# Kernel optimization log

Hardware: AMD Instinct MI355X
Metric: run time of the kernel (lower is better)

The kernel has to match this reference:

```python
import jax, jax.numpy as jnp
import numpy as np

VOCAB = 100000; E = 256; H = 256; Hh = 128; K = 12
START = 9; STOP = 10; PAD = 11; NEG = -10000.0
B = 32; T = 512


def setup_inputs() -> dict:
    key = jax.random.key(0)
    ks = jax.random.split(key, 16)
    u = 1.0 / np.sqrt(Hh)  # pytorch LSTM init scale
    xav = lambda k, shape: jax.random.normal(k, shape, jnp.float32) * np.sqrt(2.0 / (shape[0] + shape[1]))
    trans = jax.random.normal(ks[10], (K, K), jnp.float32)
    trans = trans.at[START, :].set(NEG).at[:, STOP].set(NEG)
    trans = trans.at[PAD, :].set(NEG).at[:, PAD].set(NEG)
    return {
        "sentence": jax.random.randint(ks[0], (B, T), 0, VOCAB),
        "h0": jax.random.normal(ks[1], (2, B, Hh), jnp.float32),
        "c0": jax.random.normal(ks[2], (2, B, Hh), jnp.float32),
        "embed": xav(ks[3], (VOCAB, E)),
        "W_ih_f": jax.random.uniform(ks[4], (4 * Hh, E), jnp.float32, -u, u),
        "W_hh_f": jax.random.uniform(ks[5], (4 * Hh, Hh), jnp.float32, -u, u),
        "b_f": jax.random.uniform(ks[6], (4 * Hh,), jnp.float32, -u, u),
        "W_ih_r": jax.random.uniform(ks[7], (4 * Hh, E), jnp.float32, -u, u),
        "W_hh_r": jax.random.uniform(ks[8], (4 * Hh, Hh), jnp.float32, -u, u),
        "b_r": jax.random.uniform(ks[9], (4 * Hh,), jnp.float32, -u, u),
        "W_out": xav(ks[11], (K, H)),
        "b_out": jnp.zeros((K,), jnp.float32),
        "transitions": trans,
    }


def _lstm_dir(xe, W_ih, W_hh, b, h0, c0):
    # xe: [T,B,E]; precompute input contribution once (big GEMM outside scan)
    xg = jnp.einsum('tbe,ge->tbg', xe, W_ih) + b  # [T,B,4*Hh]
    def step(carry, xt):
        h, c = carry
        g = xt + h @ W_hh.T
        i, f, gg, o = jnp.split(g, 4, axis=-1)  # pytorch gate order i,f,g,o
        c = jax.nn.sigmoid(f) * c + jax.nn.sigmoid(i) * jnp.tanh(gg)
        h = jax.nn.sigmoid(o) * jnp.tanh(c)
        return (h, c), h
    _, hs = jax.lax.scan(step, (h0, c0), xg)
    return hs  # [T,B,Hh]


def reference(sentence, h0, c0, embed, W_ih_f, W_hh_f, b_f, W_ih_r, W_hh_r, b_r,
              W_out, b_out, transitions):
    xe = embed[sentence].transpose(1, 0, 2)  # [T,B,E]
    hs_f = _lstm_dir(xe, W_ih_f, W_hh_f, b_f, h0[0], c0[0])
    hs_r = _lstm_dir(xe[::-1], W_ih_r, W_hh_r, b_r, h0[1], c0[1])[::-1]
    hs = jnp.concatenate([hs_f, hs_r], axis=-1)           # [T,B,H]
    feats = hs @ W_out.T + b_out                          # [T,B,K]

    # Viterbi max-plus recurrence
    scores0 = jnp.full((B, K), NEG, jnp.float32).at[:, START].set(0.0)
    def vstep(scores, feat):
        m = scores[:, None, :] + transitions[None, :, :]  # [B,K_next,K_prev]
        ptr = jnp.argmax(m, axis=-1).astype(jnp.int32)
        return jnp.max(m, axis=-1) + feat, ptr
    scores, pointers = jax.lax.scan(vstep, scores0, feats)  # pointers [T,B,K]
    scores = scores + transitions[STOP]
    best_tag = jnp.argmax(scores, axis=-1).astype(jnp.int32)  # [B]

    # parallel backtrace (reverse scan, outputs in original time order)
    def back(tag, ptr):
        prev = jnp.take_along_axis(ptr, tag[:, None], axis=1)[:, 0]
        return prev, tag
    _, path = jax.lax.scan(back, best_tag, pointers, reverse=True)  # [T,B]
    return path.T  # [B,T] int32 best tag sequence
```

## Files before the change

### kernel.cpp

```cpp
#include <hip/hip_runtime.h>
#include <hip/hip_bf16.h>
#include <cmath>

#define TT 512
#define BB 32
#define EE 256
#define HH 128
#define KCRF 12
#define NEGF (-10000.0f)

__global__ __launch_bounds__(256) void k1_xg(const int* __restrict__ sent,
    const float* __restrict__ embed,
    const float* __restrict__ Wf, const float* __restrict__ bf,
    const float* __restrict__ Wr, const float* __restrict__ br,
    float* __restrict__ XG)
{
  __shared__ __align__(16) float As[64][36];
  __shared__ __align__(16) float Bs[128][36];
  const int tid = threadIdx.x;
  const int m0 = (blockIdx.x >> 3) * 64;
  const int n0 = (blockIdx.x & 7) * 128;
  const int ty = tid >> 4, tx = tid & 15;
  float acc[4][8];
#pragma unroll
  for (int i = 0; i < 4; ++i)
#pragma unroll
    for (int j = 0; j < 8; ++j) acc[i][j] = 0.f;

  for (int k0 = 0; k0 < 256; k0 += 32) {
#pragma unroll
    for (int r = 0; r < 2; ++r) {
      int idx = tid + r * 256;
      int row = idx >> 3;
      int c4 = (idx & 7) << 2;
      int R = m0 + row;
      int t = R >> 5, b = R & 31;
      const float4 v = *(const float4*)(embed + (long)sent[b * TT + t] * 256 + k0 + c4);
      *(float4*)&As[row][c4] = v;
    }
#pragma unroll
    for (int r = 0; r < 4; ++r) {
      int idx = tid + r * 256;
      int row = idx >> 3;
      int c4 = (idx & 7) << 2;
      int col = n0 + row;
      const float* src = (col < 512) ? (Wf + (long)col * 256) : (Wr + (long)(col - 512) * 256);
      const float4 v = *(const float4*)(src + k0 + c4);
      *(float4*)&Bs[row][c4] = v;
    }
    __syncthreads();
#pragma unroll
    for (int kk = 0; kk < 32; ++kk) {
      float a[4], bv[8];
#pragma unroll
      for (int i = 0; i < 4; ++i) a[i] = As[ty * 4 + i][kk];
#pragma unroll
      for (int j = 0; j < 8; ++j) bv[j] = Bs[tx + 16 * j][kk];
#pragma unroll
      for (int i = 0; i < 4; ++i)
#pragma unroll
        for (int j = 0; j < 8; ++j) acc[i][j] = fmaf(a[i], bv[j], acc[i][j]);
    }
    __syncthreads();
  }
#pragma unroll
  for (int i = 0; i < 4; ++i) {
    int R = m0 + ty * 4 + i;
#pragma unroll
    for (int j = 0; j < 8; ++j) {
      int col = n0 + tx + 16 * j;
      float bias = (col < 512) ? bf[col] : br[col - 512];
      XG[(long)R * 1024 + col] = acc[i][j] + bias;
    }
  }
}

__global__ __launch_bounds__(512) __attribute__((amdgpu_waves_per_eu(1)))
void k2_scan(const float* __restrict__ XG,
    const float* __restrict__ Whf, const float* __restrict__ Whr,
    const float* __restrict__ h0, const float* __restrict__ c0,
    float* __restrict__ HS)
{
  const int wg = blockIdx.x;
  const int dir = wg >> 5;
  const int b = wg & 31;
  const int j = threadIdx.x;
  const float* Wh = dir ? Whr : Whf;

  float4 w[32];
#pragma unroll
  for (int i = 0; i < 32; ++i)
    w[i] = *(const float4*)(Wh + (long)j * 128 + i * 4);

  __shared__ __align__(16) float hs[128];
  __shared__ float gs[512];
  float c = 0.f;
  if (j < 128) {
    hs[j] = h0[(dir * 32 + b) * 128 + j];
    c = c0[(dir * 32 + b) * 128 + j];
  }
  __syncthreads();

  const int t0 = dir ? (TT - 1) : 0;
  const long stepoff = dir ? -32768 : 32768;
  const float* xp = XG + ((long)t0 * 32 + b) * 1024 + dir * 512 + j;
  float xg_cur = *xp;
  const int gate = j >> 7;

  for (int s = 0; s < TT; ++s) {
    const int t = dir ? (TT - 1 - s) : s;
    float xg_nxt = 0.f;
    if (s + 1 < TT) { xp += stepoff; xg_nxt = *xp; }

    float a0 = xg_cur, a1 = 0.f, a2 = 0.f, a3 = 0.f;
#pragma unroll
    for (int i = 0; i < 32; ++i) {
      const float4 hv = *(const float4*)(hs + 4 * i);
      a0 = fmaf(w[i].x, hv.x, a0);
      a1 = fmaf(w[i].y, hv.y, a1);
      a2 = fmaf(w[i].z, hv.z, a2);
      a3 = fmaf(w[i].w, hv.w, a3);
    }
    const float acc = (a0 + a1) + (a2 + a3);
    const float act = (gate == 2) ? tanhf(acc) : (1.f / (1.f + expf(-acc)));
    gs[j] = act;
    __syncthreads();
    if (j < 128) {
      float ig = gs[j], fg = gs[128 + j], gg = gs[256 + j], og = gs[384 + j];
      c = fmaf(fg, c, ig * gg);
      float h = og * tanhf(c);
      hs[j] = h;
      HS[((long)t * 32 + b) * 256 + dir * 128 + j] = h;
    }
    __syncthreads();
    xg_cur = xg_nxt;
  }
}

__global__ __launch_bounds__(64) void k3_feats(const float* __restrict__ HS,
    const float* __restrict__ Wout, const float* __restrict__ bout,
    float* __restrict__ FE)
{
  __shared__ __align__(16) float ws[12 * 256];
  __shared__ float bs[12];
  const int tid = threadIdx.x;
  for (int i = tid; i < 768; i += 64)
    ((float4*)ws)[i] = ((const float4*)Wout)[i];
  if (tid < 12) bs[tid] = bout[tid];
  __syncthreads();
  const long row = (long)blockIdx.x * 64 + tid;
  const float4* hp = (const float4*)(HS + row * 256);
  float acc[12];
#pragma unroll
  for (int k = 0; k < 12; ++k) acc[k] = bs[k];
  for (int e4 = 0; e4 < 64; ++e4) {
    float4 hv = hp[e4];
#pragma unroll
    for (int k = 0; k < 12; ++k) {
      const float4 wv = *(const float4*)&ws[k * 256 + e4 * 4];
      acc[k] = fmaf(hv.x, wv.x, acc[k]);
      acc[k] = fmaf(hv.y, wv.y, acc[k]);
      acc[k] = fmaf(hv.z, wv.z, acc[k]);
      acc[k] = fmaf(hv.w, wv.w, acc[k]);
    }
  }
  const int t = (int)(row >> 5), b = (int)(row & 31);
#pragma unroll
  for (int k = 0; k < 12; ++k) FE[((long)t * 12 + k) * 32 + b] = acc[k];
}

__global__ __launch_bounds__(384) void k4_viterbi(const float* __restrict__ FE,
    const float* __restrict__ trans, int* __restrict__ out)
{
  __shared__ unsigned char nib[TT * 192];
  __shared__ float sc[2][32][12];
  __shared__ float tr[144];
  __shared__ unsigned char stag[2][384];
  __shared__ int btag[32];
  const int tid = threadIdx.x;
  const int b = tid & 31, nxt = tid >> 5;
  if (tid < 144) tr[tid] = trans[tid];
  if (nxt == 0) {
#pragma unroll
    for (int p = 0; p < 12; ++p) sc[0][b][p] = (p == 9) ? 0.f : NEGF;
  }
  __syncthreads();
  float fnext = FE[nxt * 32 + b];
  for (int t = 0; t < TT; ++t) {
    const int cur = t & 1;
    const float feat = fnext;
    if (t + 1 < TT) fnext = FE[(t + 1) * 384 + nxt * 32 + b];
    float best = -1e30f; int arg = 0;
#pragma unroll
    for (int p = 0; p < 12; ++p) {
      float v = sc[cur][b][p] + tr[nxt * 12 + p];
      if (v > best) { best = v; arg = p; }
    }
    sc[cur ^ 1][b][nxt] = best + feat;
    stag[cur][b * 12 + nxt] = (unsigned char)arg;
    if (t > 0 && tid < 192) {
      const int bb = tid / 6, p = tid % 6;
      nib[(t - 1) * 192 + tid] =
          (unsigned char)(stag[cur ^ 1][bb * 12 + 2 * p] |
                          (stag[cur ^ 1][bb * 12 + 2 * p + 1] << 4));
    }
    __syncthreads();
  }
  if (tid < 192) {
    const int bb = tid / 6, p = tid % 6;
    nib[511 * 192 + tid] =
        (unsigned char)(stag[1][bb * 12 + 2 * p] | (stag[1][bb * 12 + 2 * p + 1] << 4));
  }
  if (nxt == 0) {
    float best = -1e30f; int arg = 0;
#pragma unroll
    for (int p = 0; p < 12; ++p) {
      float v = sc[0][b][p] + tr[10 * 12 + p];
      if (v > best) { best = v; arg = p; }
    }
    btag[b] = arg;
  }
  __syncthreads();
  if (tid < 32) {
    int tag = btag[b];
    for (int t = TT - 1; t >= 0; --t) {
      out[b * TT + t] = tag;
      if (t) {
        unsigned char v = nib[t * 192 + b * 6 + (tag >> 1)];
        tag = (tag & 1) ? (v >> 4) : (v & 15);
      }
    }
  }
}

extern "C" void kernel_launch(void* const* d_in, const int* in_sizes, int n_in,
                              void* d_out, int out_size, void* d_ws, size_t ws_size,
                              hipStream_t stream)
{
  const int* sent = (const int*)d_in[0];
  const float* h0 = (const float*)d_in[1];
  const float* c0 = (const float*)d_in[2];
  const float* embed = (const float*)d_in[3];
  const float* Wif = (const float*)d_in[4];
  const float* Whf = (const float*)d_in[5];
  const float* bf = (const float*)d_in[6];
  const float* Wir = (const float*)d_in[7];
  const float* Whr = (const float*)d_in[8];
  const float* br = (const float*)d_in[9];
  const float* Wout = (const float*)d_in[10];
  const float* bout = (const float*)d_in[11];
  const float* trans = (const float*)d_in[12];

  char* ws = (char*)d_ws;
  float* XG = (float*)ws;
  float* HS = (float*)(ws + 67108864);
  float* FE = (float*)(ws + 67108864 + 16777216);
  int* out = (int*)d_out;

  hipLaunchKernelGGL(k1_xg, dim3(2048), dim3(256), 0, stream,
                     sent, embed, Wif, bf, Wir, br, XG);
  hipLaunchKernelGGL(k2_scan, dim3(64), dim3(512), 0, stream,
                     XG, Whf, Whr, h0, c0, HS);
  hipLaunchKernelGGL(k3_feats, dim3(256), dim3(64), 0, stream,
                     HS, Wout, bout, FE);
  hipLaunchKernelGGL(k4_viterbi, dim3(1), dim3(384), 0, stream,
                     FE, trans, out);
}
```

Before: 809.5 us.

## Process two batch rows per LSTM scan workgroup to reuse register weights

The recurrent LSTM kernel now handles two batch elements per workgroup, so each thread's register-resident W_hh row is applied to two hidden vectors per step. This halves the grid from 64 to 32 workgroups and doubles the FMA work per thread per step. The barrier count per step stays the same but is shared across two sequences. The gain depends on whether per-step latency is set by barriers and the activation and LDS path rather than by FMA throughput, and the smaller grid leaves more CUs idle.

Result: slower. 1.880 ms (+132.3%).

```diff
diff --git a/kernel.cpp b/kernel.cpp
--- a/kernel.cpp
+++ b/kernel.cpp
@@ -75,65 +75,85 @@
   }
 }
 
-__global__ __launch_bounds__(512) __attribute__((amdgpu_waves_per_eu(1)))
+__global__ __launch_bounds__(512, 2)
 void k2_scan(const float* __restrict__ XG,
     const float* __restrict__ Whf, const float* __restrict__ Whr,
     const float* __restrict__ h0, const float* __restrict__ c0,
     float* __restrict__ HS)
 {
   const int wg = blockIdx.x;
-  const int dir = wg >> 5;
-  const int b = wg & 31;
+  const int dir = wg >> 4;
+  const int b1 = wg & 15;
+  const int b2 = b1 + 16;
   const int j = threadIdx.x;
   const float* Wh = dir ? Whr : Whf;
 
   float4 w[32];
 #pragma unroll
   for (int i = 0; i < 32; ++i)
-    w[i] = *(const float4*)(Wh + (long)j * 128 + i * 4);
-
-  __shared__ __align__(16) float hs[128];
-  __shared__ float gs[512];
+    w[i] = *(const float4*)(Wh + (long)j * 128 + 4 * i);
+
+  __shared__ __align__(16) float hs[2][128];
+  __shared__ float gs[2][512];
   float c = 0.f;
   if (j < 128) {
-    hs[j] = h0[(dir * 32 + b) * 128 + j];
-    c = c0[(dir * 32 + b) * 128 + j];
+    hs[0][j] = h0[(dir * 32 + b1) * 128 + j];
+    c = c0[(dir * 32 + b1) * 128 + j];
+  } else if (j < 256) {
+    hs[1][j - 128] = h0[(dir * 32 + b2) * 128 + (j - 128)];
+    c = c0[(dir * 32 + b2) * 128 + (j - 128)];
   }
   __syncthreads();
 
   const int t0 = dir ? (TT - 1) : 0;
   const long stepoff = dir ? -32768 : 32768;
-  const float* xp = XG + ((long)t0 * 32 + b) * 1024 + dir * 512 + j;
-  float xg_cur = *xp;
+  const float* xp1 = XG + ((long)t0 * 32 + b1) * 1024 + dir * 512 + j;
+  const float* xp2 = XG + ((long)t0 * 32 + b2) * 1024 + dir * 512 + j;
+  float xg1 = *xp1, xg2 = *xp2;
   const int gate = j >> 7;
 
   for (int s = 0; s < TT; ++s) {
     const int t = dir ? (TT - 1 - s) : s;
-    float xg_nxt = 0.f;
-    if (s + 1 < TT) { xp += stepoff; xg_nxt = *xp; }
-
-    float a0 = xg_cur, a1 = 0.f, a2 = 0.f, a3 = 0.f;
+    float nx1 = 0.f, nx2 = 0.f;
+    if (s + 1 < TT) {
+      xp1 += stepoff; nx1 = *xp1;
+      xp2 += stepoff; nx2 = *xp2;
+    }
+
+    float a0 = xg1, a1 = 0.f, a2 = 0.f, a3 = 0.f;
+    float d0 = xg2, d1 = 0.f, d2 = 0.f, d3 = 0.f;
 #pragma unroll
     for (int i = 0; i < 32; ++i) {
-      const float4 hv = *(const float4*)(hs + 4 * i);
-      a0 = fmaf(w[i].x, hv.x, a0);
-      a1 = fmaf(w[i].y, hv.y, a1);
-      a2 = fmaf(w[i].z, hv.z, a2);
-      a3 = fmaf(w[i].w, hv.w, a3);
-    }
-    const float acc = (a0 + a1) + (a2 + a3);
-    const float act = (gate == 2) ? tanhf(acc) : (1.f / (1.f + expf(-acc)));
-    gs[j] = act;
-    __syncthreads();
-    if (j < 128) {
-      float ig = gs[j], fg = gs[128 + j], gg = gs[256 + j], og = gs[384 + j];
+      const float4 h1 = *(const float4*)(hs[0] + 4 * i);
+      const float4 h2 = *(const float4*)(hs[1] + 4 * i);
+      a0 = fmaf(w[i].x, h1.x, a0);
+      a1 = fmaf(w[i].y, h1.y, a1);
+      a2 = fmaf(w[i].z, h1.z, a2);
+      a3 = fmaf(w[i].w, h1.w, a3);
+      d0 = fmaf(w[i].x, h2.x, d0);
+      d1 = fmaf(w[i].y, h2.y, d1);
+      d2 = fmaf(w[i].z, h2.z, d2);
+      d3 = fmaf(w[i].w, h2.w, d3);
+    }
+    const float acc1 = (a0 + a1) + (a2 + a3);
+    const float acc2 = (d0 + d1) + (d2 + d3);
+    const float act1 = (gate == 2) ? tanhf(acc1) : (1.f / (1.f + expf(-acc1)));
+    const float act2 = (gate == 2) ? tanhf(acc2) : (1.f / (1.f + expf(-acc2)));
+    gs[0][j] = act1;
+    gs[1][j] = act2;
+    __syncthreads();
+    if (j < 256) {
+      const int bb = j >> 7;
+      const int d = j & 127;
+      const float ig = gs[bb][d], fg = gs[bb][128 + d];
+      const float gg = gs[bb][256 + d], og = gs[bb][384 + d];
       c = fmaf(fg, c, ig * gg);
-      float h = og * tanhf(c);
-      hs[j] = h;
-      HS[((long)t * 32 + b) * 256 + dir * 128 + j] = h;
-    }
-    __syncthreads();
-    xg_cur = xg_nxt;
+      const float h = og * tanhf(c);
+      hs[bb][d] = h;
+      HS[((long)t * 32 + (bb ? b2 : b1)) * 256 + dir * 128 + d] = h;
+    }
+    __syncthreads();
+    xg1 = nx1; xg2 = nx2;
   }
 }
 
@@ -259,7 +279,7 @@
 
   hipLaunchKernelGGL(k1_xg, dim3(2048), dim3(256), 0, stream,
                      sent, embed, Wif, bf, Wir, br, XG);
-  hipLaunchKernelGGL(k2_scan, dim3(64), dim3(512), 0, stream,
+  hipLaunchKernelGGL(k2_scan, dim3(32), dim3(512), 0, stream,
                      XG, Whf, Whr, h0, c0, HS);
   hipLaunchKernelGGL(k3_feats, dim3(256), dim3(64), 0, stream,
                      HS, Wout, bout, FE);
```

## Split Viterbi across blocks with wave-local shuffles instead of block barriers

Applied to the files above, without the earlier changes.

The Viterbi kernel moves from one 384-thread block to 8 single-wave blocks, each handling 4 batch rows with 16-lane groups. Per-step score exchange goes through __shfl within a 16-lane group, which removes the per-timestep __syncthreads and the shared-memory score arrays. Backpointers are stored as plain bytes rather than packed nibbles. In exchange, each wave does 12 serial shuffles per step and the FE loads are strided.

Measured after the change: 838.2 us. +3.5%, slower.

```diff
diff --git a/kernel.cpp b/kernel.cpp
--- a/kernel.cpp
+++ b/kernel.cpp
@@ -169,66 +169,51 @@
   for (int k = 0; k < 12; ++k) FE[((long)t * 12 + k) * 32 + b] = acc[k];
 }
 
-__global__ __launch_bounds__(384) void k4_viterbi(const float* __restrict__ FE,
+__global__ __launch_bounds__(64) void k4_viterbi(const float* __restrict__ FE,
     const float* __restrict__ trans, int* __restrict__ out)
 {
-  __shared__ unsigned char nib[TT * 192];
-  __shared__ float sc[2][32][12];
-  __shared__ float tr[144];
-  __shared__ unsigned char stag[2][384];
-  __shared__ int btag[32];
-  const int tid = threadIdx.x;
-  const int b = tid & 31, nxt = tid >> 5;
-  if (tid < 144) tr[tid] = trans[tid];
-  if (nxt == 0) {
-#pragma unroll
-    for (int p = 0; p < 12; ++p) sc[0][b][p] = (p == 9) ? 0.f : NEGF;
+  __shared__ unsigned char ptrl[TT * 48];
+  const int lane = threadIdx.x;
+  const int p = lane >> 4;
+  const int l = lane & 15;
+  const int b = blockIdx.x * 4 + p;
+  const int nxt = (l < 12) ? l : 0;
+
+  float tr[12];
+#pragma unroll
+  for (int q = 0; q < 12; ++q) tr[q] = trans[nxt * 12 + q];
+  const float trStop = trans[10 * 12 + nxt];
+
+  float s = (nxt == 9 && l < 12) ? 0.f : NEGF;
+  float fnext = FE[(0 * 12 + nxt) * 32 + b];
+
+  for (int t = 0; t < TT; ++t) {
+    const float feat = fnext;
+    if (t + 1 < TT) fnext = FE[((t + 1) * 12 + nxt) * 32 + b];
+    float best = -1e30f; int arg = 0;
+#pragma unroll
+    for (int q = 0; q < 12; ++q) {
+      const float sq = __shfl(s, q, 16);
+      const float v = sq + tr[q];
+      if (v > best) { best = v; arg = q; }
+    }
+    s = best + feat;
+    if (l < 12) ptrl[t * 48 + p * 12 + l] = (unsigned char)arg;
+  }
+
+  const float sf = s + trStop;
+  float best = -1e30f; int arg = 0;
+#pragma unroll
+  for (int q = 0; q < 12; ++q) {
+    const float v = __shfl(sf, q, 16);
+    if (v > best) { best = v; arg = q; }
   }
   __syncthreads();
-  float fnext = FE[nxt * 32 + b];
-  for (int t = 0; t < TT; ++t) {
-    const int cur = t & 1;
-    const float feat = fnext;
-    if (t + 1 < TT) fnext = FE[(t + 1) * 384 + nxt * 32 + b];
-    float best = -1e30f; int arg = 0;
-#pragma unroll
-    for (int p = 0; p < 12; ++p) {
-      float v = sc[cur][b][p] + tr[nxt * 12 + p];
-      if (v > best) { best = v; arg = p; }
-    }
-    sc[cur ^ 1][b][nxt] = best + feat;
-    stag[cur][b * 12 + nxt] = (unsigned char)arg;
-    if (t > 0 && tid < 192) {
-      const int bb = tid / 6, p = tid % 6;
-      nib[(t - 1) * 192 + tid] =
-          (unsigned char)(stag[cur ^ 1][bb * 12 + 2 * p] |
-                          (stag[cur ^ 1][bb * 12 + 2 * p + 1] << 4));
-    }
-    __syncthreads();
-  }
-  if (tid < 192) {
-    const int bb = tid / 6, p = tid % 6;
-    nib[511 * 192 + tid] =
-        (unsigned char)(stag[1][bb * 12 + 2 * p] | (stag[1][bb * 12 + 2 * p + 1] << 4));
-  }
-  if (nxt == 0) {
-    float best = -1e30f; int arg = 0;
-#pragma unroll
-    for (int p = 0; p < 12; ++p) {
-      float v = sc[0][b][p] + tr[10 * 12 + p];
-      if (v > best) { best = v; arg = p; }
-    }
-    btag[b] = arg;
-  }
-  __syncthreads();
-  if (tid < 32) {
-    int tag = btag[b];
+  if (l == 0) {
+    int tag = arg;
     for (int t = TT - 1; t >= 0; --t) {
       out[b * TT + t] = tag;
-      if (t) {
-        unsigned char v = nib[t * 192 + b * 6 + (tag >> 1)];
-        tag = (tag & 1) ? (v >> 4) : (v & 15);
-      }
+      if (t) tag = ptrl[t * 48 + p * 12 + tag];
     }
   }
 }
@@ -263,6 +248,6 @@
                      XG, Whf, Whr, h0, c0, HS);
   hipLaunchKernelGGL(k3_feats, dim3(256), dim3(64), 0, stream,
                      HS, Wout, bout, FE);
-  hipLaunchKernelGGL(k4_viterbi, dim3(1), dim3(384), 0, stream,
+  hipLaunchKernelGGL(k4_viterbi, dim3(8), dim3(64), 0, stream,
                      FE, trans, out);
 }
```
